# Optimization experiments

Hardware: AMD Instinct MI355X
Metric: run time of the kernel (lower is better)

The kernel has to match this reference:

```python
import jax, jax.numpy as jnp
import numpy as np

B, C, G, P, W, H = 16, 64, 256, 4096, 1024, 256
WQ = W // 4  # wsi_dim // 4 = 256
D = C + G + WQ  # concat dim fed to score MLP = 576


def _init_linear(key, fan_in, fan_out):
    k1, k2 = jax.random.split(key)
    bound = 1.0 / np.sqrt(fan_in)
    w = jax.random.uniform(k1, (fan_in, fan_out), jnp.float32, -bound, bound)
    b = jax.random.uniform(k2, (fan_out,), jnp.float32, -bound, bound)
    return w, b


def setup_inputs() -> dict:
    key = jax.random.key(0)
    ks = jax.random.split(key, 8)
    cx = jax.random.normal(ks[0], (B, C), jnp.float32)
    gx = jax.random.normal(ks[1], (B, G), jnp.float32)
    wx = jax.random.normal(ks[2], (B, P, W), jnp.float32)
    Wc, bc = _init_linear(ks[3], C, C)        # fc_c
    Wg, bg = _init_linear(ks[4], G, G)        # fc_g
    Ww, bw = _init_linear(ks[5], W, WQ)       # fc_w
    W1, b1 = _init_linear(ks[6], D, H)        # FCLayers hidden
    W2, b2 = _init_linear(ks[7], H, 1)        # FCLayers out
    return {"cx": cx, "gx": gx, "wx": wx,
            "Wc": Wc, "bc": bc, "Wg": Wg, "bg": bg, "Ww": Ww, "bw": bw,
            "W1": W1, "b1": b1, "W2": W2, "b2": b2}


def reference(cx, gx, wx, Wc, bc, Wg, bg, Ww, bw, W1, b1, W2, b2):
    # Per-modality projections
    c = cx @ Wc + bc                      # [B, C]
    g = gx @ Wg + bg                      # [B, G]
    w = jnp.einsum('bpw,wq->bpq', wx, Ww) + bw  # [B, P, WQ]
    # Score MLP on concat(c, g, w_i) for every patch, vectorized by
    # splitting W1 rows over the concat blocks (avoids materializing concat):
    W1c, W1g, W1w = W1[:C], W1[C:C + G], W1[C + G:]
    h = jax.nn.relu((c @ W1c + g @ W1g + b1)[:, None, :]
                    + jnp.einsum('bpq,qh->bph', w, W1w))  # [B, P, H]
    scores = h @ W2 + b2                  # [B, P, 1]
    attn = jax.nn.softmax(scores, axis=1)  # softmax over patches
    return jnp.sum(attn * w, axis=1)      # [B, WQ]
```

## Files before the change

kernel.cpp:

```cpp
#include <hip/hip_runtime.h>
#include <hip/hip_bf16.h>

#define B_   16
#define C_   64
#define G_   256
#define P_   4096
#define W_   1024
#define H_   256
#define WQ_  256
#define M_   (B_ * P_)

typedef __attribute__((ext_vector_type(8))) _Float16 f16x8;
typedef __attribute__((ext_vector_type(4))) float    f32x4;

__device__ __forceinline__ float h2f(ushort u) {
    union { ushort u; _Float16 h; } cv; cv.u = u;
    return (float)cv.h;
}

__global__ __launch_bounds__(256) void convT16_kernel(
    const float* __restrict__ src, ushort* __restrict__ dst, int K, int N)
{
    __shared__ float tile[64][65];
    const int nb = N >> 6;
    const int k0 = (blockIdx.x / nb) * 64;
    const int n0 = (blockIdx.x % nb) * 64;
    const int t = threadIdx.x;
    #pragma unroll
    for (int i = 0; i < 16; ++i) {
        int e = i * 256 + t;
        int kr = e >> 6, nc = e & 63;
        tile[nc][kr] = src[(size_t)(k0 + kr) * N + n0 + nc];
    }
    __syncthreads();
    #pragma unroll
    for (int i = 0; i < 16; ++i) {
        int e = i * 256 + t;
        int nc = e >> 6, kr = e & 63;
        union { _Float16 h; ushort u; } cv;
        cv.h = (_Float16)tile[nc][kr];
        dst[(size_t)(n0 + nc) * K + k0 + kr] = cv.u;
    }
}

__global__ __launch_bounds__(256) void prep_kernel(
    const float* __restrict__ cx, const float* __restrict__ gx,
    const float* __restrict__ Wc, const float* __restrict__ bc,
    const float* __restrict__ Wg, const float* __restrict__ bg,
    const float* __restrict__ W1, const float* __restrict__ b1,
    float* __restrict__ base_out)
{
    const int b = blockIdx.x;
    const int t = threadIdx.x;
    __shared__ float cxl[C_], gxl[G_], cl[C_], gl[G_];

    if (t < C_) cxl[t] = cx[b * C_ + t];
    gxl[t] = gx[b * G_ + t];
    __syncthreads();

    if (t < C_) {
        float acc = bc[t];
        #pragma unroll 4
        for (int i = 0; i < C_; ++i) acc += cxl[i] * Wc[i * C_ + t];
        cl[t] = acc;
    }
    {
        float acc = bg[t];
        #pragma unroll 4
        for (int i = 0; i < G_; ++i) acc += gxl[i] * Wg[i * G_ + t];
        gl[t] = acc;
    }
    __syncthreads();

    float acc = b1[t];
    #pragma unroll 4
    for (int i = 0; i < C_; ++i) acc += cl[i] * W1[i * H_ + t];
    #pragma unroll 4
    for (int i = 0; i < G_; ++i) acc += gl[i] * W1[(C_ + i) * H_ + t];
    base_out[b * H_ + t] = acc;
}

__global__ __launch_bounds__(512, 2) void gemm_w_mfma(
    const float* __restrict__ A,
    const ushort* __restrict__ BT,
    const float* __restrict__ bw,
    ushort* __restrict__ Cout)
{
    __shared__ __align__(16) ushort Ah[128 * 64];
    __shared__ __align__(16) ushort Bh[256 * 64];
    const int t = threadIdx.x;
    const int row0 = blockIdx.x * 128;
    const int lane = t & 63, wave = t >> 6;
    const int wm = wave >> 2, wn = wave & 3;
    const int l15 = lane & 15, lq = lane >> 4;

    const int s_ar = t >> 2;
    const int s_ak = (t & 3) * 16;
    const int s_bc = t >> 1;
    const int s_bk = (t & 1) * 32;

    f32x4 acc[4][4];
    #pragma unroll
    for (int m = 0; m < 4; ++m)
        #pragma unroll
        for (int n = 0; n < 4; ++n) acc[m][n] = (f32x4){0.f, 0.f, 0.f, 0.f};

    for (int k0 = 0; k0 < W_; k0 += 64) {
        if (k0) __syncthreads();
        {
            const float* ap = A + (size_t)(row0 + s_ar) * W_ + k0 + s_ak;
            const float4 v0 = *(const float4*)(ap + 0);
            const float4 v1 = *(const float4*)(ap + 4);
            const float4 v2 = *(const float4*)(ap + 8);
            const float4 v3 = *(const float4*)(ap + 12);
            f16x8 h0, h1;
            h0[0] = (_Float16)v0.x; h0[1] = (_Float16)v0.y;
            h0[2] = (_Float16)v0.z; h0[3] = (_Float16)v0.w;
            h0[4] = (_Float16)v1.x; h0[5] = (_Float16)v1.y;
            h0[6] = (_Float16)v1.z; h0[7] = (_Float16)v1.w;
            h1[0] = (_Float16)v2.x; h1[1] = (_Float16)v2.y;
            h1[2] = (_Float16)v2.z; h1[3] = (_Float16)v2.w;
            h1[4] = (_Float16)v3.x; h1[5] = (_Float16)v3.y;
            h1[6] = (_Float16)v3.z; h1[7] = (_Float16)v3.w;
            const int base = s_ar * 128 + s_ak * 2;
            const int swz  = (s_ar & 7) << 4;
            *(f16x8*)((char*)Ah + (base ^ swz)) = h0;
            *(f16x8*)((char*)Ah + ((base + 16) ^ swz)) = h1;
        }
        #pragma unroll
        for (int i = 0; i < 4; ++i) {
            const int kk = s_bk + i * 8;
            const int byte = (s_bc * 128 + kk * 2) ^ ((s_bc & 7) << 4);
            *(uint4*)((char*)Bh + byte) =
                *(const uint4*)(BT + (size_t)s_bc * W_ + k0 + kk);
        }
        __syncthreads();

        #pragma unroll
        for (int ks = 0; ks < 2; ++ks) {
            f16x8 af[4], bf[4];
            #pragma unroll
            for (int m = 0; m < 4; ++m) {
                const int r = wm * 64 + m * 16 + l15;
                const int byte = (r * 128 + ks * 64 + lq * 16) ^ ((r & 7) << 4);
                af[m] = *(const f16x8*)((const char*)Ah + byte);
            }
            #pragma unroll
            for (int n = 0; n < 4; ++n) {
                const int c = wn * 64 + n * 16 + l15;
                const int byte = (c * 128 + ks * 64 + lq * 16) ^ ((c & 7) << 4);
                bf[n] = *(const f16x8*)((const char*)Bh + byte);
            }
            #pragma unroll
            for (int m = 0; m < 4; ++m)
                #pragma unroll
                for (int n = 0; n < 4; ++n)
                    acc[m][n] = __builtin_amdgcn_mfma_f32_16x16x32_f16(
                        af[m], bf[n], acc[m][n], 0, 0, 0);
        }
    }

    float bwv[4];
    #pragma unroll
    for (int n = 0; n < 4; ++n) bwv[n] = bw[wn * 64 + n * 16 + l15];
    #pragma unroll
    for (int m = 0; m < 4; ++m)
        #pragma unroll
        for (int reg = 0; reg < 4; ++reg) {
            const size_t r = (size_t)row0 + wm * 64 + m * 16 + lq * 4 + reg;
            #pragma unroll
            for (int n = 0; n < 4; ++n) {
                union { _Float16 h; ushort u; } cv;
                cv.h = (_Float16)(acc[m][n][reg] + bwv[n]);
                Cout[r * WQ_ + wn * 64 + n * 16 + l15] = cv.u;
            }
        }
}

__global__ __launch_bounds__(512) void gemm_scores_mfma(
    const ushort* __restrict__ A16,
    const ushort* __restrict__ BT,
    const float* __restrict__ base_,
    const float* __restrict__ W2,
    const float* __restrict__ b2,
    float* __restrict__ scores)
{
    __shared__ __align__(16) ushort Ah[128 * 32];
    __shared__ __align__(16) ushort Bh[256 * 32];
    __shared__ float red[4][128];
    const int t = threadIdx.x;
    const int row0 = blockIdx.x * 128;
    const int b = blockIdx.x >> 5;
    const int lane = t & 63, wave = t >> 6;
    const int wm = wave >> 2, wn = wave & 3;
    const int l15 = lane & 15, lq = lane >> 4;

    const int sa_r = t >> 2;
    const int sa_k = (t & 3) * 8;
    const int sb_c = t >> 1;
    const int sb_k = (t & 1) * 16;

    f32x4 acc[4][4];
    #pragma unroll
    for (int m = 0; m < 4; ++m)
        #pragma unroll
        for (int n = 0; n < 4; ++n) acc[m][n] = (f32x4){0.f, 0.f, 0.f, 0.f};

    for (int k0 = 0; k0 < H_; k0 += 32) {
        if (k0) __syncthreads();
        {
            const int bytea = (sa_r * 64 + sa_k * 2) ^ ((sa_r & 7) << 4);
            *(uint4*)((char*)Ah + bytea) =
                *(const uint4*)(A16 + (size_t)(row0 + sa_r) * H_ + k0 + sa_k);
        }
        {
            const int byteb0 = (sb_c * 64 + sb_k * 2) ^ ((sb_c & 7) << 4);
            const int byteb1 = (sb_c * 64 + sb_k * 2 + 16) ^ ((sb_c & 7) << 4);
            *(uint4*)((char*)Bh + byteb0) =
                *(const uint4*)(BT + (size_t)sb_c * H_ + k0 + sb_k);
            *(uint4*)((char*)Bh + byteb1) =
                *(const uint4*)(BT + (size_t)sb_c * H_ + k0 + sb_k + 8);
        }
        __syncthreads();

        f16x8 af[4], bf[4];
        #pragma unroll
        for (int m = 0; m < 4; ++m) {
            const int r = wm * 64 + m * 16 + l15;
            const int byte = (r * 64 + lq * 16) ^ ((r & 7) << 4);
            af[m] = *(const f16x8*)((const char*)Ah + byte);
        }
        #pragma unroll
        for (int n = 0; n < 4; ++n) {
            const int c = wn * 64 + n * 16 + l15;
            const int byte = (c * 64 + lq * 16) ^ ((c & 7) << 4);
            bf[n] = *(const f16x8*)((const char*)Bh + byte);
        }
        #pragma unroll
        for (int m = 0; m < 4; ++m)
            #pragma unroll
            for (int n = 0; n < 4; ++n)
                acc[m][n] = __builtin_amdgcn_mfma_f32_16x16x32_f16(
                    af[m], bf[n], acc[m][n], 0, 0, 0);
    }

    float basev[4], w2v[4];
    #pragma unroll
    for (int n = 0; n < 4; ++n) {
        const int col = wn * 64 + n * 16 + l15;
        basev[n] = base_[b * H_ + col];
        w2v[n] = W2[col];
    }
    __syncthreads();
    #pragma unroll
    for (int m = 0; m < 4; ++m)
        #pragma unroll
        for (int reg = 0; reg < 4; ++reg) {
            float s = 0.f;
            #pragma unroll
            for (int n = 0; n < 4; ++n) {
                float h = acc[m][n][reg] + basev[n];
                h = fmaxf(h, 0.f);
                s += h * w2v[n];
            }
            s += __shfl_xor(s, 1, 64);
            s += __shfl_xor(s, 2, 64);
            s += __shfl_xor(s, 4, 64);
            s += __shfl_xor(s, 8, 64);
            if (l15 == 0) red[wn][wm * 64 + m * 16 + lq * 4 + reg] = s;
        }
    __syncthreads();
    if (t < 128) {
        scores[row0 + t] = red[0][t] + red[1][t] + red[2][t] + red[3][t] + b2[0];
    }
}

__global__ __launch_bounds__(256) void softmax_stats_kernel(
    const float* __restrict__ scores, float* __restrict__ mz)
{
    const int b = blockIdx.x;
    const int t = threadIdx.x;
    __shared__ float red[8];

    float m = -1e30f;
    for (int p = t; p < P_; p += 256) m = fmaxf(m, scores[b * P_ + p]);
    #pragma unroll
    for (int d = 1; d < 64; d <<= 1) m = fmaxf(m, __shfl_xor(m, d, 64));
    if ((t & 63) == 0) red[t >> 6] = m;
    __syncthreads();
    if (t == 0) red[4] = fmaxf(fmaxf(red[0], red[1]), fmaxf(red[2], red[3]));
    __syncthreads();
    m = red[4];
    __syncthreads();

    float z = 0.f;
    for (int p = t; p < P_; p += 256) z += expf(scores[b * P_ + p] - m);
    #pragma unroll
    for (int d = 1; d < 64; d <<= 1) z += __shfl_xor(z, d, 64);
    if ((t & 63) == 0) red[t >> 6] = z;
    __syncthreads();
    if (t == 0) { mz[2 * b] = m; mz[2 * b + 1] = red[0] + red[1] + red[2] + red[3]; }
}

__global__ __launch_bounds__(256) void weighted_partial_kernel(
    const ushort* __restrict__ wmat16, const float* __restrict__ scores,
    const float* __restrict__ mz, float* __restrict__ part)
{
    const int blk = blockIdx.x;
    const int b   = blk >> 5;
    const int sl  = blk & 31;
    const int t   = threadIdx.x;
    const int rg  = t >> 5;
    const int q8  = (t & 31) * 8;
    const float m = mz[2 * b];
    __shared__ float red[8][WQ_];

    float acc[8];
    #pragma unroll
    for (int j = 0; j < 8; ++j) acc[j] = 0.f;

    const int p0 = sl * 128 + rg * 16;
    for (int p = p0; p < p0 + 16; ++p) {
        const float e = expf(scores[b * P_ + p] - m);
        const uint4 raw = *(const uint4*)(wmat16 + ((size_t)b * P_ + p) * WQ_ + q8);
        const ushort* u = (const ushort*)&raw;
        #pragma unroll
        for (int j = 0; j < 8; ++j) acc[j] += e * h2f(u[j]);
    }
    #pragma unroll
    for (int j = 0; j < 8; ++j) red[rg][q8 + j] = acc[j];
    __syncthreads();
    float s = 0.f;
    #pragma unroll
    for (int g = 0; g < 8; ++g) s += red[g][t];
    part[(size_t)(b * 32 + sl) * WQ_ + t] = s;
}

__global__ __launch_bounds__(256) void finalize_kernel(
    const float* __restrict__ part, const float* __restrict__ mz,
    float* __restrict__ out)
{
    const int b = blockIdx.x;
    const int t = threadIdx.x;
    const float z = mz[2 * b + 1];
    float acc = 0.f;
    #pragma unroll
    for (int sl = 0; sl < 32; ++sl) acc += part[(size_t)(b * 32 + sl) * WQ_ + t];
    out[b * WQ_ + t] = acc / z;
}

extern "C" void kernel_launch(void* const* d_in, const int* in_sizes, int n_in,
                              void* d_out, int out_size, void* d_ws, size_t ws_size,
                              hipStream_t stream) {
    const float* cx = (const float*)d_in[0];
    const float* gx = (const float*)d_in[1];
    const float* wx = (const float*)d_in[2];
    const float* Wc = (const float*)d_in[3];
    const float* bc = (const float*)d_in[4];
    const float* Wg = (const float*)d_in[5];
    const float* bg = (const float*)d_in[6];
    const float* Ww = (const float*)d_in[7];
    const float* bw = (const float*)d_in[8];
    const float* W1 = (const float*)d_in[9];
    const float* b1 = (const float*)d_in[10];
    const float* W2 = (const float*)d_in[11];
    const float* b2 = (const float*)d_in[12];
    float* out = (float*)d_out;

    float* ws        = (float*)d_ws;
    ushort* ws_w16   = (ushort*)ws;
    float* ws_scores = ws + (size_t)M_ * WQ_ / 2;
    float* ws_base   = ws_scores + M_;
    float* ws_mz     = ws_base + B_ * H_;
    float* ws_part   = ws_mz + 2 * B_;
    ushort* WwT16    = (ushort*)(ws_part + B_ * 32 * WQ_);
    ushort* W1T16    = WwT16 + (size_t)W_ * WQ_;

    convT16_kernel<<<(W_ / 64) * (WQ_ / 64), 256, 0, stream>>>(Ww, WwT16, W_, WQ_);
    convT16_kernel<<<(H_ / 64) * (H_ / 64), 256, 0, stream>>>(
        W1 + (size_t)(C_ + G_) * H_, W1T16, H_, H_);

    prep_kernel<<<B_, 256, 0, stream>>>(cx, gx, Wc, bc, Wg, bg, W1, b1, ws_base);

    gemm_w_mfma<<<M_ / 128, 512, 0, stream>>>(wx, WwT16, bw, ws_w16);

    gemm_scores_mfma<<<M_ / 128, 512, 0, stream>>>(
        ws_w16, W1T16, ws_base, W2, b2, ws_scores);

    softmax_stats_kernel<<<B_, 256, 0, stream>>>(ws_scores, ws_mz);

    weighted_partial_kernel<<<B_ * 32, 256, 0, stream>>>(ws_w16, ws_scores, ws_mz, ws_part);

    finalize_kernel<<<B_, 256, 0, stream>>>(ws_part, ws_mz, out);
}
```

Before: 187.2 us.

## Fuse score GEMM into projection GEMM kernel, reading fp16 tile back from global

Merges the wx@Ww projection kernel and the score MLP GEMM into one kernel. Each block writes its fp16 projected tile, fences, syncs, then reads the tile and W1T straight from global/L2 into MFMA fragments without LDS staging. This removes one launch and lets the second GEMM hit L2 on freshly written data. The risk is uncoalesced, unstaged global fragment loads in the inner loop and more register pressure in the fused kernel.

```diff
diff --git a/kernel.cpp b/kernel.cpp
--- a/kernel.cpp
+++ b/kernel.cpp
@@ -80,16 +80,23 @@
     base_out[b * H_ + t] = acc;
 }
 
-__global__ __launch_bounds__(512, 2) void gemm_w_mfma(
+__global__ __launch_bounds__(512, 2) void gemm_w_fused(
     const float* __restrict__ A,
     const ushort* __restrict__ BT,
     const float* __restrict__ bw,
-    ushort* __restrict__ Cout)
+    const ushort* __restrict__ W1T,
+    const float* __restrict__ base_,
+    const float* __restrict__ W2,
+    const float* __restrict__ b2,
+    ushort* __restrict__ Cout,
+    float* __restrict__ scores)
 {
     __shared__ __align__(16) ushort Ah[128 * 64];
     __shared__ __align__(16) ushort Bh[256 * 64];
+    __shared__ float red2[4][128];
     const int t = threadIdx.x;
     const int row0 = blockIdx.x * 128;
+    const int b = blockIdx.x >> 5;
     const int lane = t & 63, wave = t >> 6;
     const int wm = wave >> 2, wn = wave & 3;
     const int l15 = lane & 15, lq = lane >> 4;
@@ -160,118 +167,83 @@
         }
     }
 
-    float bwv[4];
-    #pragma unroll
-    for (int n = 0; n < 4; ++n) bwv[n] = bw[wn * 64 + n * 16 + l15];
+    {
+        float bwv[4];
+        #pragma unroll
+        for (int n = 0; n < 4; ++n) bwv[n] = bw[wn * 64 + n * 16 + l15];
+        #pragma unroll
+        for (int m = 0; m < 4; ++m)
+            #pragma unroll
+            for (int reg = 0; reg < 4; ++reg) {
+                const size_t r = (size_t)row0 + wm * 64 + m * 16 + lq * 4 + reg;
+                #pragma unroll
+                for (int n = 0; n < 4; ++n) {
+                    union { _Float16 h; ushort u; } cv;
+                    cv.h = (_Float16)(acc[m][n][reg] + bwv[n]);
+                    Cout[r * WQ_ + wn * 64 + n * 16 + l15] = cv.u;
+                }
+            }
+    }
+
+    __threadfence();
+    __syncthreads();
+
+    f32x4 acc2[4][4];
     #pragma unroll
     for (int m = 0; m < 4; ++m)
         #pragma unroll
-        for (int reg = 0; reg < 4; ++reg) {
-            const size_t r = (size_t)row0 + wm * 64 + m * 16 + lq * 4 + reg;
-            #pragma unroll
-            for (int n = 0; n < 4; ++n) {
-                union { _Float16 h; ushort u; } cv;
-                cv.h = (_Float16)(acc[m][n][reg] + bwv[n]);
-                Cout[r * WQ_ + wn * 64 + n * 16 + l15] = cv.u;
-            }
-        }
-}
-
-__global__ __launch_bounds__(512) void gemm_scores_mfma(
-    const ushort* __restrict__ A16,
-    const ushort* __restrict__ BT,
-    const float* __restrict__ base_,
-    const float* __restrict__ W2,
-    const float* __restrict__ b2,
-    float* __restrict__ scores)
-{
-    __shared__ __align__(16) ushort Ah[128 * 32];
-    __shared__ __align__(16) ushort Bh[256 * 32];
-    __shared__ float red[4][128];
-    const int t = threadIdx.x;
-    const int row0 = blockIdx.x * 128;
-    const int b = blockIdx.x >> 5;
-    const int lane = t & 63, wave = t >> 6;
-    const int wm = wave >> 2, wn = wave & 3;
-    const int l15 = lane & 15, lq = lane >> 4;
-
-    const int sa_r = t >> 2;
-    const int sa_k = (t & 3) * 8;
-    const int sb_c = t >> 1;
-    const int sb_k = (t & 1) * 16;
-
-    f32x4 acc[4][4];
-    #pragma unroll
-    for (int m = 0; m < 4; ++m)
-        #pragma unroll
-        for (int n = 0; n < 4; ++n) acc[m][n] = (f32x4){0.f, 0.f, 0.f, 0.f};
-
-    for (int k0 = 0; k0 < H_; k0 += 32) {
-        if (k0) __syncthreads();
-        {
-            const int bytea = (sa_r * 64 + sa_k * 2) ^ ((sa_r & 7) << 4);
-            *(uint4*)((char*)Ah + bytea) =
-                *(const uint4*)(A16 + (size_t)(row0 + sa_r) * H_ + k0 + sa_k);
-        }
-        {
-            const int byteb0 = (sb_c * 64 + sb_k * 2) ^ ((sb_c & 7) << 4);
-            const int byteb1 = (sb_c * 64 + sb_k * 2 + 16) ^ ((sb_c & 7) << 4);
-            *(uint4*)((char*)Bh + byteb0) =
-                *(const uint4*)(BT + (size_t)sb_c * H_ + k0 + sb_k);
-            *(uint4*)((char*)Bh + byteb1) =
-                *(const uint4*)(BT + (size_t)sb_c * H_ + k0 + sb_k + 8);
-        }
-        __syncthreads();
-
+        for (int n = 0; n < 4; ++n) acc2[m][n] = (f32x4){0.f, 0.f, 0.f, 0.f};
+
+    for (int k2 = 0; k2 < WQ_; k2 += 32) {
         f16x8 af[4], bf[4];
         #pragma unroll
         for (int m = 0; m < 4; ++m) {
-            const int r = wm * 64 + m * 16 + l15;
-            const int byte = (r * 64 + lq * 16) ^ ((r & 7) << 4);
-            af[m] = *(const f16x8*)((const char*)Ah + byte);
+            const size_t r = (size_t)row0 + wm * 64 + m * 16 + l15;
+            af[m] = *(const f16x8*)(Cout + r * WQ_ + k2 + lq * 8);
         }
         #pragma unroll
         for (int n = 0; n < 4; ++n) {
             const int c = wn * 64 + n * 16 + l15;
-            const int byte = (c * 64 + lq * 16) ^ ((c & 7) << 4);
-            bf[n] = *(const f16x8*)((const char*)Bh + byte);
+            bf[n] = *(const f16x8*)(W1T + (size_t)c * WQ_ + k2 + lq * 8);
         }
         #pragma unroll
         for (int m = 0; m < 4; ++m)
             #pragma unroll
             for (int n = 0; n < 4; ++n)
-                acc[m][n] = __builtin_amdgcn_mfma_f32_16x16x32_f16(
-                    af[m], bf[n], acc[m][n], 0, 0, 0);
-    }
-
-    float basev[4], w2v[4];
-    #pragma unroll
-    for (int n = 0; n < 4; ++n) {
-        const int col = wn * 64 + n * 16 + l15;
-        basev[n] = base_[b * H_ + col];
-        w2v[n] = W2[col];
-    }
-    __syncthreads();
-    #pragma unroll
-    for (int m = 0; m < 4; ++m)
-        #pragma unroll
-        for (int reg = 0; reg < 4; ++reg) {
-            float s = 0.f;
-            #pragma unroll
-            for (int n = 0; n < 4; ++n) {
-                float h = acc[m][n][reg] + basev[n];
-                h = fmaxf(h, 0.f);
-                s += h * w2v[n];
+                acc2[m][n] = __builtin_amdgcn_mfma_f32_16x16x32_f16(
+                    af[m], bf[n], acc2[m][n], 0, 0, 0);
+    }
+
+    {
+        float basev[4], w2v[4];
+        #pragma unroll
+        for (int n = 0; n < 4; ++n) {
+            const int col = wn * 64 + n * 16 + l15;
+            basev[n] = base_[b * H_ + col];
+            w2v[n] = W2[col];
+        }
+        #pragma unroll
+        for (int m = 0; m < 4; ++m)
+            #pragma unroll
+            for (int reg = 0; reg < 4; ++reg) {
+                float s = 0.f;
+                #pragma unroll
+                for (int n = 0; n < 4; ++n) {
+                    float h = acc2[m][n][reg] + basev[n];
+                    h = fmaxf(h, 0.f);
+                    s += h * w2v[n];
+                }
+                s += __shfl_xor(s, 1, 64);
+                s += __shfl_xor(s, 2, 64);
+                s += __shfl_xor(s, 4, 64);
+                s += __shfl_xor(s, 8, 64);
+                if (l15 == 0) red2[wn][wm * 64 + m * 16 + lq * 4 + reg] = s;
             }
-            s += __shfl_xor(s, 1, 64);
-            s += __shfl_xor(s, 2, 64);
-            s += __shfl_xor(s, 4, 64);
-            s += __shfl_xor(s, 8, 64);
-            if (l15 == 0) red[wn][wm * 64 + m * 16 + lq * 4 + reg] = s;
-        }
-    __syncthreads();
-    if (t < 128) {
-        scores[row0 + t] = red[0][t] + red[1][t] + red[2][t] + red[3][t] + b2[0];
+        __syncthreads();
+        if (t < 128) {
+            scores[row0 + t] =
+                red2[0][t] + red2[1][t] + red2[2][t] + red2[3][t] + b2[0];
+        }
     }
 }
 
@@ -382,10 +354,8 @@
 
     prep_kernel<<<B_, 256, 0, stream>>>(cx, gx, Wc, bc, Wg, bg, W1, b1, ws_base);
 
-    gemm_w_mfma<<<M_ / 128, 512, 0, stream>>>(wx, WwT16, bw, ws_w16);
-
-    gemm_scores_mfma<<<M_ / 128, 512, 0, stream>>>(
-        ws_w16, W1T16, ws_base, W2, b2, ws_scores);
+    gemm_w_fused<<<M_ / 128, 512, 0, stream>>>(
+        wx, WwT16, bw, W1T16, ws_base, W2, b2, ws_w16, ws_scores);
 
     softmax_stats_kernel<<<B_, 256, 0, stream>>>(ws_scores, ws_mz);
 
```

New measurement: 352.9 us. 88.5% more time.
